# Kernel tuning notes

Measured on AMD Instinct MI355X. Metric: run time of the kernel, lower is better.

Reference implementation:

```python
import jax, jax.numpy as jnp
import numpy as np

B, N, FD, FH, FW = 2, 6, 256, 28, 60
DIM, HEADS, DH = 128, 4, 32
BH, BW = 50, 50
IMG_H, IMG_W = 224, 480
SCALE = DH ** -0.5


def _ln(t, g, b):
    m = t.mean(-1, keepdims=True)
    v = jnp.mean((t - m) ** 2, -1, keepdims=True)
    return (t - m) / jnp.sqrt(v + 1e-5) * g + b


def _bn_relu(t, g, b, m, v):
    # eval-mode BatchNorm2d over channel axis 2 of (b,n,C,h,w), then ReLU
    sh = (1, 1, -1, 1, 1)
    y = (t - m.reshape(sh)) / jnp.sqrt(v.reshape(sh) + 1e-5) * g.reshape(sh) + b.reshape(sh)
    return jax.nn.relu(y)


def setup_inputs():
    key = jax.random.key(0)
    it = iter(jax.random.split(key, 48))
    def rn(shape, s=1.0):
        return s * jax.random.normal(next(it), shape, dtype=jnp.float32)
    # BEVEmbedding.grid buffer: V_inv @ scaled unit grid (first 2 rows used)
    gx, gy = np.meshgrid(np.linspace(0, 1, BW), np.linspace(0, 1, BH))
    grid = np.stack([gx * 200.0, gy * 200.0, np.ones_like(gx)], 0)
    V = np.array([[0.0, -2.0, 100.0], [-2.0, 0.0, 100.0], [0.0, 0.0, 1.0]])
    g = np.linalg.inv(V) @ grid.reshape(3, -1)
    bev_grid = jnp.asarray(g[:2].reshape(2, BH, BW), jnp.float32)
    # image_plane buffer, flattened to (3, fh*fw)
    px, py = np.meshgrid(np.linspace(0, 1, FW) * IMG_W, np.linspace(0, 1, FH) * IMG_H)
    image_plane = jnp.asarray(np.stack([px, py, np.ones_like(px)], 0).reshape(3, -1), jnp.float32)
    ones = jnp.ones(DIM, jnp.float32)
    zeros = jnp.zeros(DIM, jnp.float32)
    return dict(
        x=rn((B, DIM, BH, BW)),
        feature=rn((B, N, FD, FH, FW)),
        I_inv=rn((B, N, 3, 3), 0.01) + jnp.eye(3, dtype=jnp.float32),
        E_inv=rn((B, N, 4, 4), 0.1) + jnp.eye(4, dtype=jnp.float32),
        bev_grid=bev_grid, image_plane=image_plane,
        W_cam=rn((DIM, 4), 0.1), W_img=rn((DIM, 4), 0.1),
        W_bev=rn((DIM, 2), 0.1), b_bev=rn((DIM,), 0.1),
        fp_bn_g=jnp.ones(FD, jnp.float32), fp_bn_b=jnp.zeros(FD, jnp.float32),
        fp_bn_m=rn((FD,), 0.1), fp_bn_v=jax.random.uniform(next(it), (FD,), jnp.float32, 0.5, 1.5),
        fl_bn_g=jnp.ones(FD, jnp.float32), fl_bn_b=jnp.zeros(FD, jnp.float32),
        fl_bn_m=rn((FD,), 0.1), fl_bn_v=jax.random.uniform(next(it), (FD,), jnp.float32, 0.5, 1.5),
        W_fproj=rn((DIM, FD), 0.05), W_flin=rn((DIM, FD), 0.05),
        q_ln_g=ones, q_ln_b=zeros, Wq=rn((HEADS * DH, DIM), 0.05), bq=zeros,
        k_ln_g=ones, k_ln_b=zeros, Wk=rn((HEADS * DH, DIM), 0.05), bk=zeros,
        v_ln_g=ones, v_ln_b=zeros, Wv=rn((HEADS * DH, DIM), 0.05), bv=zeros,
        Wproj=rn((DIM, HEADS * DH), 0.05), bproj=zeros,
        pre_ln_g=ones, pre_ln_b=zeros,
        mlp_W1=rn((2 * DIM, DIM), 0.05), mlp_b1=jnp.zeros(2 * DIM, jnp.float32),
        mlp_W2=rn((DIM, 2 * DIM), 0.05), mlp_b2=zeros,
        post_ln_g=ones, post_ln_b=zeros,
    )


def reference(x, feature, I_inv, E_inv, bev_grid, image_plane, W_cam, W_img, W_bev, b_bev,
              fp_bn_g, fp_bn_b, fp_bn_m, fp_bn_v, fl_bn_g, fl_bn_b, fl_bn_m, fl_bn_v,
              W_fproj, W_flin, q_ln_g, q_ln_b, Wq, bq, k_ln_g, k_ln_b, Wk, bk,
              v_ln_g, v_ln_b, Wv, bv, Wproj, bproj, pre_ln_g, pre_ln_b,
              mlp_W1, mlp_b1, mlp_W2, mlp_b2, post_ln_g, post_ln_b):
    b, n, _, fh, fw = feature.shape
    H, W = x.shape[2], x.shape[3]
    Q, K = H * W, fh * fw
    # camera-center embedding: 1x1 conv on E_inv translation column (b,n,4)
    c_embed = jnp.einsum('dc,bnc->bnd', W_cam, E_inv[..., 3])
    # per-pixel ray directions: E_inv @ pad(I_inv @ pixel, 1)
    cam = jnp.einsum('bnij,jp->bnip', I_inv, image_plane)                 # (b,n,3,K)
    cam = jnp.concatenate([cam, jnp.ones_like(cam[:, :, :1])], axis=2)    # (b,n,4,K)
    d = jnp.einsum('bnij,bnjp->bnip', E_inv, cam)                         # (b,n,4,K)
    img = jnp.einsum('dc,bncp->bndp', W_img, d) - c_embed[..., None]      # (b,n,dim,K)
    img = img / (jnp.linalg.norm(img, axis=2, keepdims=True) + 1e-7)
    # BEV positional embedding (1x1 conv with bias on world grid)
    w_embed = jnp.einsum('dc,chw->dhw', W_bev, bev_grid) + b_bev[:, None, None]
    bev_e = w_embed[None, None] - c_embed[..., None, None]                # (b,n,dim,H,W)
    bev_e = bev_e / (jnp.linalg.norm(bev_e, axis=2, keepdims=True) + 1e-7)
    # key/value features: BN(eval)+ReLU+1x1 conv
    key_feat = jnp.einsum('dc,bnchw->bndhw', W_fproj, _bn_relu(feature, fp_bn_g, fp_bn_b, fp_bn_m, fp_bn_v))
    key = img.reshape(b, n, -1, fh, fw) + key_feat                        # (b,n,dim,fh,fw)
    val = jnp.einsum('dc,bnchw->bndhw', W_flin, _bn_relu(feature, fl_bn_g, fl_bn_b, fl_bn_m, fl_bn_v))
    query = bev_e + x[:, None]                                            # (b,n,dim,H,W)
    # CrossAttention: LN + linear projections
    qx = query.reshape(b, n, -1, Q).transpose(0, 1, 3, 2)                 # (b,n,Q,dim)
    kx = key.reshape(b, n, -1, K).transpose(0, 1, 3, 2)                   # (b,n,K,dim)
    vx = val.reshape(b, n, -1, K).transpose(0, 1, 3, 2).reshape(b, n * K, -1)
    qh = (_ln(qx, q_ln_g, q_ln_b) @ Wq.T + bq).reshape(b, n, Q, HEADS, DH)
    kh = (_ln(kx, k_ln_g, k_ln_b) @ Wk.T + bk).reshape(b, n, K, HEADS, DH)
    vh = (_ln(vx, v_ln_g, v_ln_b) @ Wv.T + bv).reshape(b, n * K, HEADS, DH)
    # scores per view, softmax over flattened (n K) key axis
    dot = SCALE * jnp.einsum('bnqmd,bnkmd->bmqnk', qh, kh)                # (b,m,Q,n,K)
    att = jax.nn.softmax(dot.reshape(b, HEADS, Q, n * K), axis=-1)
    a = jnp.einsum('bmqk,bkmd->bqmd', att, vh).reshape(b, Q, HEADS * DH)
    z = a @ Wproj.T + bproj
    z = z + x.reshape(b, -1, Q).transpose(0, 2, 1)                        # skip connection
    z = _ln(z, pre_ln_g, pre_ln_b)
    z = z + (jax.nn.gelu(z @ mlp_W1.T + mlp_b1, approximate=False) @ mlp_W2.T + mlp_b2)
    z = _ln(z, post_ln_g, post_ln_b)
    return z.transpose(0, 2, 1).reshape(b, -1, H, W)
```

## Files before the change

### kernel.cpp

```cpp
#include <hip/hip_runtime.h>

#define NB    2
#define NCAM  6
#define FD    256
#define KK    1680
#define DIMN  128
#define NHEAD 4
#define DHD   32
#define QQ    2500
#define SCALE 0.17677669529663687f
#define QSCALE ((float)(0.17677669529663687 * 1.4426950408889634))

typedef short bf8 __attribute__((ext_vector_type(8)));
typedef float f4  __attribute__((ext_vector_type(4)));

__device__ __forceinline__ unsigned short f2bf(float f) {
  unsigned int u = __float_as_uint(f);
  unsigned int r = (u + 0x7fffu + ((u >> 16) & 1u)) >> 16;
  return (unsigned short)r;
}

__device__ __forceinline__ float blk_sum128(float v, float* red) {
  #pragma unroll
  for (int o = 32; o > 0; o >>= 1) v += __shfl_down(v, o);
  int t = threadIdx.x;
  if ((t & 63) == 0) red[t >> 6] = v;
  __syncthreads();
  float r = red[0] + red[1];
  __syncthreads();
  return r;
}

__global__ void k_cembed(const float* __restrict__ W_cam, const float* __restrict__ E_inv,
                         float* __restrict__ ce) {
  int bn = blockIdx.x;
  int d  = threadIdx.x;
  const float* e = E_inv + bn * 16;
  float s = 0.f;
  #pragma unroll
  for (int c = 0; c < 4; ++c) s += W_cam[d * 4 + c] * e[c * 4 + 3];
  ce[bn * 128 + d] = s;
}

__global__ void k_img(const float* __restrict__ I_inv, const float* __restrict__ E_inv,
                      const float* __restrict__ plane, const float* __restrict__ W_img,
                      const float* __restrict__ ce, float* __restrict__ key) {
  __shared__ float red[2];
  int p  = blockIdx.x;
  int bn = blockIdx.y;
  int d  = threadIdx.x;
  const float* Ii = I_inv + bn * 9;
  const float* Ei = E_inv + bn * 16;
  float pl0 = plane[p], pl1 = plane[KK + p], pl2 = plane[2 * KK + p];
  float c0 = Ii[0]*pl0 + Ii[1]*pl1 + Ii[2]*pl2;
  float c1 = Ii[3]*pl0 + Ii[4]*pl1 + Ii[5]*pl2;
  float c2 = Ii[6]*pl0 + Ii[7]*pl1 + Ii[8]*pl2;
  float d0 = Ei[0]*c0 + Ei[1]*c1 + Ei[2]*c2  + Ei[3];
  float d1 = Ei[4]*c0 + Ei[5]*c1 + Ei[6]*c2  + Ei[7];
  float d2 = Ei[8]*c0 + Ei[9]*c1 + Ei[10]*c2 + Ei[11];
  float d3 = Ei[12]*c0 + Ei[13]*c1 + Ei[14]*c2 + Ei[15];
  float v = W_img[d*4]*d0 + W_img[d*4+1]*d1 + W_img[d*4+2]*d2 + W_img[d*4+3]*d3
            - ce[bn * 128 + d];
  float ss = blk_sum128(v * v, red);
  float inv = 1.f / (sqrtf(ss) + 1e-7f);
  key[((size_t)bn * KK + p) * DIMN + d] = v * inv;
}

__global__ void k_query(const float* __restrict__ bev_grid, const float* __restrict__ W_bev,
                        const float* __restrict__ b_bev, const float* __restrict__ ce,
                        const float* __restrict__ x, float* __restrict__ query) {
  __shared__ float red[2];
  int q  = blockIdx.x;
  int bn = blockIdx.y;
  int b  = bn / NCAM;
  int d  = threadIdx.x;
  float g0 = bev_grid[q], g1 = bev_grid[QQ + q];
  float v = W_bev[d * 2] * g0 + W_bev[d * 2 + 1] * g1 + b_bev[d] - ce[bn * 128 + d];
  float ss = blk_sum128(v * v, red);
  float inv = 1.f / (sqrtf(ss) + 1e-7f);
  query[((size_t)bn * QQ + q) * DIMN + d] = v * inv + x[(size_t)(b * DIMN + d) * QQ + q];
}

#define TP 16
__global__ void k_featconv(const float* __restrict__ feat,
                           const float* __restrict__ g1c, const float* __restrict__ b1c,
                           const float* __restrict__ m1c, const float* __restrict__ v1c,
                           const float* __restrict__ g2c, const float* __restrict__ b2c,
                           const float* __restrict__ m2c, const float* __restrict__ v2c,
                           const float* __restrict__ Wfp, const float* __restrict__ Wfl,
                           float* __restrict__ key, float* __restrict__ val) {
  __shared__ float sc1[FD], sh1[FD], sc2[FD], sh2[FD];
  __shared__ float t1[FD * (TP + 1)];
  __shared__ float t2[FD * (TP + 1)];
  int tile = blockIdx.x;
  int bn   = blockIdx.y;
  int t    = threadIdx.x;
  int p0   = tile * TP;
  {
    int c = t;
    float s1 = g1c[c] * rsqrtf(v1c[c] + 1e-5f);
    sc1[c] = s1; sh1[c] = b1c[c] - m1c[c] * s1;
    float s2 = g2c[c] * rsqrtf(v2c[c] + 1e-5f);
    sc2[c] = s2; sh2[c] = b2c[c] - m2c[c] * s2;
  }
  __syncthreads();
  const float* fb = feat + (size_t)bn * FD * KK + p0;
  int pp = t & 15, crow = t >> 4;
  #pragma unroll
  for (int i = 0; i < 16; ++i) {
    int c = i * 16 + crow;
    float raw = fb[(size_t)c * KK + pp];
    t1[c * (TP + 1) + pp] = fmaxf(raw * sc1[c] + sh1[c], 0.f);
    t2[c * (TP + 1) + pp] = fmaxf(raw * sc2[c] + sh2[c], 0.f);
  }
  __syncthreads();
  int dd = t & 127;
  const float4* W4 = (const float4*)((t < 128) ? Wfp : Wfl) + dd * 64;
  const float* tl = (t < 128) ? t1 : t2;
  float acc[TP];
  #pragma unroll
  for (int p = 0; p < TP; ++p) acc[p] = 0.f;
  for (int c4 = 0; c4 < 64; ++c4) {
    float4 w = W4[c4];
    const float* r0 = &tl[(c4 * 4 + 0) * (TP + 1)];
    const float* r1 = &tl[(c4 * 4 + 1) * (TP + 1)];
    const float* r2 = &tl[(c4 * 4 + 2) * (TP + 1)];
    const float* r3 = &tl[(c4 * 4 + 3) * (TP + 1)];
    #pragma unroll
    for (int p = 0; p < TP; ++p)
      acc[p] += w.x * r0[p] + w.y * r1[p] + w.z * r2[p] + w.w * r3[p];
  }
  __syncthreads();
  {
    float* dst = (t < 128) ? t1 : t2;
    #pragma unroll
    for (int p = 0; p < TP; ++p) dst[dd * (TP + 1) + p] = acc[p];
  }
  __syncthreads();
  #pragma unroll
  for (int i = 0; i < 16; ++i) {
    int e   = i * 256 + t;
    int ddo = e & 127, po = (e >> 7) & 15, wh = e >> 11;
    size_t addr = ((size_t)bn * KK + p0 + po) * DIMN + ddo;
    float vv = (wh ? t2 : t1)[ddo * (TP + 1) + po];
    if (wh) val[addr] = vv;
    else    key[addr] += vv;
  }
}

#define ROWS 8
template<int MODE>
__global__ void k_lnproj_bf(const float* __restrict__ in, const float* __restrict__ lng,
                            const float* __restrict__ lnb, const float* __restrict__ W,
                            const float* __restrict__ bias, unsigned short* __restrict__ out,
                            float scale) {
  __shared__ float red[2];
  __shared__ float ln[ROWS][DIMN];
  __shared__ float stats[ROWS][2];
  size_t r0 = (size_t)blockIdx.x * ROWS;
  int t = threadIdx.x;
  float g = lng[t], bb = lnb[t];
  float xv[ROWS];
  #pragma unroll
  for (int r = 0; r < ROWS; ++r) xv[r] = in[(r0 + r) * DIMN + t];
  #pragma unroll
  for (int r = 0; r < ROWS; ++r) {
    float s  = blk_sum128(xv[r], red);
    float s2 = blk_sum128(xv[r] * xv[r], red);
    if (t == 0) { stats[r][0] = s * (1.f / 128.f); stats[r][1] = s2 * (1.f / 128.f); }
  }
  __syncthreads();
  #pragma unroll
  for (int r = 0; r < ROWS; ++r) {
    float mu  = stats[r][0];
    float var = fmaxf(stats[r][1] - mu * mu, 0.f);
    float rin = rsqrtf(var + 1e-5f);
    ln[r][t] = (xv[r] - mu) * rin * g + bb;
  }
  __syncthreads();
  float acc[ROWS];
  float bv = bias[t];
  #pragma unroll
  for (int r = 0; r < ROWS; ++r) acc[r] = bv;
  const float4* W4 = (const float4*)W + t * 32;
  for (int j4 = 0; j4 < 32; ++j4) {
    float4 w = W4[j4];
    #pragma unroll
    for (int r = 0; r < ROWS; ++r)
      acc[r] += w.x * ln[r][j4*4] + w.y * ln[r][j4*4+1] + w.z * ln[r][j4*4+2] + w.w * ln[r][j4*4+3];
  }
  if (MODE == 0) {
    #pragma unroll
    for (int r = 0; r < ROWS; ++r) out[(r0 + r) * DIMN + t] = f2bf(acc[r] * scale);
  } else {
    int bn = (int)(r0 / KK), k0 = (int)(r0 % KK);
    int m = t >> 5, d = t & 31;
    unsigned int u0 = (unsigned int)f2bf(acc[0]) | ((unsigned int)f2bf(acc[1]) << 16);
    unsigned int u1 = (unsigned int)f2bf(acc[2]) | ((unsigned int)f2bf(acc[3]) << 16);
    unsigned int u2 = (unsigned int)f2bf(acc[4]) | ((unsigned int)f2bf(acc[5]) << 16);
    unsigned int u3 = (unsigned int)f2bf(acc[6]) | ((unsigned int)f2bf(acc[7]) << 16);
    uint4 pk = make_uint4(u0, u1, u2, u3);
    *(uint4*)&out[((size_t)((bn * 4 + m) * 32 + d)) * KK + k0] = pk;
  }
}

#define AW 8
#define NCHUNK 53
#define THR 8.0f
__global__ __launch_bounds__(512)
void k_attn_mfma(const unsigned short* __restrict__ qhB, const unsigned short* __restrict__ khB,
                 const unsigned short* __restrict__ vhB, float* __restrict__ aout) {
  __shared__ unsigned short pls[AW][16 * 40];
  __shared__ float lds_o[AW][16][32];
  __shared__ float lds_m[AW][16], lds_l[AW][16];
  int qt = blockIdx.x, m = blockIdx.y, b = blockIdx.z;
  int t = threadIdx.x;
  int w = t >> 6, l = t & 63;
  int c = l & 15, g = l >> 4;
  int q0 = qt * 16;

  bf8 qf[NCAM];
  #pragma unroll
  for (int n = 0; n < NCAM; ++n) {
    int q = q0 + c;
    if (q < QQ)
      qf[n] = *(const bf8*)&qhB[((size_t)(b * NCAM + n) * QQ + q) * DIMN + m * DHD + g * 8];
    else
      qf[n] = (bf8)0;
  }
  const f4 z4 = {0.f, 0.f, 0.f, 0.f};
  f4 o0 = z4, o1 = z4;
  float mrun[4], lp[4];
  #pragma unroll
  for (int i = 0; i < 4; ++i) { mrun[i] = -1e30f; lp[i] = 0.f; }

  for (int n = 0; n < NCAM; ++n) {
    const unsigned short* kb = khB + (size_t)(b * NCAM + n) * KK * DIMN + m * DHD;
    const unsigned short* vb = vhB + (size_t)((b * NCAM + n) * NHEAD + m) * DHD * KK;
    bf8 qa = qf[n];
    for (int j = w; j < NCHUNK; j += AW) {
      int k0 = j * 32;
      bool tail = (j == NCHUNK - 1);
      bf8 kf0 = *(const bf8*)&kb[(size_t)(k0 + c) * DIMN + g * 8];
      bf8 vf0 = *(const bf8*)&vb[(size_t)c * KK + k0 + g * 8];
      bf8 vf1 = *(const bf8*)&vb[(size_t)(16 + c) * KK + k0 + g * 8];
      f4 s0 = __builtin_amdgcn_mfma_f32_16x16x32_bf16(qa, kf0, z4, 0, 0, 0);
      f4 s1;
      if (!tail) {
        bf8 kf1 = *(const bf8*)&kb[(size_t)(k0 + 16 + c) * DIMN + g * 8];
        s1 = __builtin_amdgcn_mfma_f32_16x16x32_bf16(qa, kf1, z4, 0, 0, 0);
      } else {
        s1 = (f4){-1e30f, -1e30f, -1e30f, -1e30f};
      }
      float lm[4];
      #pragma unroll
      for (int i = 0; i < 4; ++i) lm[i] = fmaxf(s0[i], s1[i]);
      bool ok = (lm[0] <= mrun[0] + THR) && (lm[1] <= mrun[1] + THR)
             && (lm[2] <= mrun[2] + THR) && (lm[3] <= mrun[3] + THR);
      if (!__all(ok)) {
        #pragma unroll
        for (int i = 0; i < 4; ++i) {
          float tm = lm[i];
          #pragma unroll
          for (int msk = 1; msk < 16; msk <<= 1) tm = fmaxf(tm, __shfl_xor(tm, msk, 16));
          float mn = fmaxf(mrun[i], tm);
          float al = __builtin_amdgcn_exp2f(mrun[i] - mn);
          mrun[i] = mn;
          lp[i] *= al;
          o0[i] *= al; o1[i] *= al;
        }
      }
      #pragma unroll
      for (int i = 0; i < 4; ++i) {
        float p0 = __builtin_amdgcn_exp2f(s0[i] - mrun[i]);
        float p1 = __builtin_amdgcn_exp2f(s1[i] - mrun[i]);
        lp[i] += p0 + p1;
        pls[w][(4 * g + i) * 40 + c]      = f2bf(p0);
        pls[w][(4 * g + i) * 40 + 16 + c] = f2bf(p1);
      }
      bf8 pa = *(const bf8*)&pls[w][c * 40 + g * 8];
      o0 = __builtin_amdgcn_mfma_f32_16x16x32_bf16(pa, vf0, o0, 0, 0, 0);
      o1 = __builtin_amdgcn_mfma_f32_16x16x32_bf16(pa, vf1, o1, 0, 0, 0);
    }
  }
  #pragma unroll
  for (int i = 0; i < 4; ++i) {
    #pragma unroll
    for (int msk = 1; msk < 16; msk <<= 1) lp[i] += __shfl_xor(lp[i], msk, 16);
  }
  #pragma unroll
  for (int i = 0; i < 4; ++i) {
    int qr = 4 * g + i;
    if (c == 0) { lds_m[w][qr] = mrun[i]; lds_l[w][qr] = lp[i]; }
    lds_o[w][qr][c]      = o0[i];
    lds_o[w][qr][16 + c] = o1[i];
  }
  __syncthreads();
  {
    int q = t >> 5, d = t & 31;
    float mg = -1e30f;
    #pragma unroll
    for (int ww = 0; ww < AW; ++ww) mg = fmaxf(mg, lds_m[ww][q]);
    float lg = 0.f, og = 0.f;
    #pragma unroll
    for (int ww = 0; ww < AW; ++ww) {
      float sc = __builtin_amdgcn_exp2f(lds_m[ww][q] - mg);
      lg += lds_l[ww][q] * sc;
      og += lds_o[ww][q][d] * sc;
    }
    int qq = q0 + q;
    if (qq < QQ)
      aout[((size_t)b * QQ + qq) * DIMN + m * DHD + d] = og / lg;
  }
}

#define EQ 16
#define EPAD 4
__global__ __launch_bounds__(256)
void k_epi2(const float* __restrict__ a, const float* __restrict__ x,
            const float* __restrict__ Wproj, const float* __restrict__ bproj,
            const float* __restrict__ preg, const float* __restrict__ preb,
            const float* __restrict__ W1, const float* __restrict__ b1,
            const float* __restrict__ W2, const float* __restrict__ b2,
            const float* __restrict__ postg, const float* __restrict__ postb,
            float* __restrict__ out) {
  __shared__ float sa[EQ][DIMN + EPAD];
  __shared__ float sx[EQ][DIMN + EPAD];
  __shared__ float sln[EQ][DIMN + EPAD];
  __shared__ float sh[EQ][2 * DIMN];
  __shared__ float stats[EQ][2];
  int q0 = blockIdx.x * EQ;
  int b  = blockIdx.y;
  int t  = threadIdx.x;
  int d  = t & 127, rg = t >> 7;

  #pragma unroll
  for (int i = 0; i < 8; ++i) {
    int e = i * 256 + t;
    int q = e >> 7, dd = e & 127;
    int qq = q0 + q;
    sa[q][dd] = (qq < QQ) ? a[((size_t)b * QQ + qq) * DIMN + dd] : 0.f;
  }
  #pragma unroll
  for (int i = 0; i < 8; ++i) {
    int e = i * 256 + t;
    int dd = e >> 4, qi = e & 15;
    int qq = q0 + qi;
    sx[qi][dd] = (qq < QQ) ? x[((size_t)b * DIMN + dd) * QQ + qq] : 0.f;
  }
  __syncthreads();

  float z[8];
  {
    const float4* Wp = (const float4*)Wproj + d * 32;
    float bp = bproj[d];
    #pragma unroll
    for (int r = 0; r < 8; ++r) z[r] = bp + sx[rg * 8 + r][d];
    for (int c4 = 0; c4 < 32; ++c4) {
      float4 w = Wp[c4];
      #pragma unroll
      for (int r = 0; r < 8; ++r) {
        float4 av = *(const float4*)&sa[rg * 8 + r][c4 * 4];
        z[r] += w.x * av.x + w.y * av.y + w.z * av.z + w.w * av.w;
      }
    }
  }
  __syncthreads();
  #pragma unroll
  for (int r = 0; r < 8; ++r) sx[rg * 8 + r][d] = z[r];
  __syncthreads();
  {
    int rt = t >> 4, lane = t & 15;
    float s = 0.f, s2 = 0.f;
    #pragma unroll
    for (int j = 0; j < 8; ++j) { float v = sx[rt][lane + 16 * j]; s += v; s2 += v * v; }
    #pragma unroll
    for (int msk = 1; msk < 16; msk <<= 1) { s += __shfl_xor(s, msk, 16); s2 += __shfl_xor(s2, msk, 16); }
    if (lane == 0) { stats[rt][0] = s * (1.f / 128.f); stats[rt][1] = s2 * (1.f / 128.f); }
  }
  __syncthreads();
  float ln1[8];
  {
    float pg = preg[d], pb = preb[d];
    #pragma unroll
    for (int r = 0; r < 8; ++r) {
      int rr = rg * 8 + r;
      float mu  = stats[rr][0];
      float var = fmaxf(stats[rr][1] - mu * mu, 0.f);
      ln1[r] = (z[r] - mu) * rsqrtf(var + 1e-5f) * pg + pb;
      sln[rr][d] = ln1[r];
    }
  }
  __syncthreads();
  {
    const float4* W1p = (const float4*)W1 + t * 32;
    float hb = b1[t];
    float h[16];
    #pragma unroll
    for (int r = 0; r < 16; ++r) h[r] = hb;
    for (int c4 = 0; c4 < 32; ++c4) {
      float4 w = W1p[c4];
      #pragma unroll
      for (int r = 0; r < 16; ++r) {
        float4 lv = *(const float4*)&sln[r][c4 * 4];
        h[r] += w.x * lv.x + w.y * lv.y + w.z * lv.z + w.w * lv.w;
      }
    }
    #pragma unroll
    for (int r = 0; r < 16; ++r) {
      float hv = h[r];
      sh[r][t] = 0.5f * hv * (1.f + erff(hv * 0.70710678118f));
    }
  }
  __syncthreads();
  float o[8];
  {
    const float4* W2p = (const float4*)W2 + d * 64;
    float b2v = b2[d];
    #pragma unroll
    for (int r = 0; r < 8; ++r) o[r] = ln1[r] + b2v;
    for (int c4 = 0; c4 < 64; ++c4) {
      float4 w = W2p[c4];
      #pragma unroll
      for (int r = 0; r < 8; ++r) {
        float4 hv = *(const float4*)&sh[rg * 8 + r][c4 * 4];
        o[r] += w.x * hv.x + w.y * hv.y + w.z * hv.z + w.w * hv.w;
      }
    }
  }
  __syncthreads();
  #pragma unroll
  for (int r = 0; r < 8; ++r) sx[rg * 8 + r][d] = o[r];
  __syncthreads();
  {
    int rt = t >> 4, lane = t & 15;
    float s = 0.f, s2 = 0.f;
    #pragma unroll
    for (int j = 0; j < 8; ++j) { float v = sx[rt][lane + 16 * j]; s += v; s2 += v * v; }
    #pragma unroll
    for (int msk = 1; msk < 16; msk <<= 1) { s += __shfl_xor(s, msk, 16); s2 += __shfl_xor(s2, msk, 16); }
    if (lane == 0) { stats[rt][0] = s * (1.f / 128.f); stats[rt][1] = s2 * (1.f / 128.f); }
  }
  __syncthreads();
  {
    float pg = postg[d], pb = postb[d];
    #pragma unroll
    for (int r = 0; r < 8; ++r) {
      int rr = rg * 8 + r;
      float mu  = stats[rr][0];
      float var = fmaxf(stats[rr][1] - mu * mu, 0.f);
      sa[rr][d] = (o[r] - mu) * rsqrtf(var + 1e-5f) * pg + pb;
    }
  }
  __syncthreads();
  #pragma unroll
  for (int i = 0; i < 8; ++i) {
    int e = i * 256 + t;
    int dd = e >> 4, qi = e & 15;
    int qq = q0 + qi;
    if (qq < QQ) out[((size_t)b * DIMN + dd) * QQ + qq] = sa[qi][dd];
  }
}

extern "C" void kernel_launch(void* const* d_in, const int* in_sizes, int n_in,
                              void* d_out, int out_size, void* d_ws, size_t ws_size,
                              hipStream_t stream) {
  const float* x        = (const float*)d_in[0];
  const float* feature  = (const float*)d_in[1];
  const float* I_inv    = (const float*)d_in[2];
  const float* E_inv    = (const float*)d_in[3];
  const float* bev_grid = (const float*)d_in[4];
  const float* plane    = (const float*)d_in[5];
  const float* W_cam    = (const float*)d_in[6];
  const float* W_img    = (const float*)d_in[7];
  const float* W_bev    = (const float*)d_in[8];
  const float* b_bev    = (const float*)d_in[9];
  const float* fp_g = (const float*)d_in[10];
  const float* fp_b = (const float*)d_in[11];
  const float* fp_m = (const float*)d_in[12];
  const float* fp_v = (const float*)d_in[13];
  const float* fl_g = (const float*)d_in[14];
  const float* fl_b = (const float*)d_in[15];
  const float* fl_m = (const float*)d_in[16];
  const float* fl_v = (const float*)d_in[17];
  const float* W_fproj = (const float*)d_in[18];
  const float* W_flin  = (const float*)d_in[19];
  const float* q_ln_g = (const float*)d_in[20];
  const float* q_ln_b = (const float*)d_in[21];
  const float* Wq = (const float*)d_in[22];
  const float* bq = (const float*)d_in[23];
  const float* k_ln_g = (const float*)d_in[24];
  const float* k_ln_b = (const float*)d_in[25];
  const float* Wk = (const float*)d_in[26];
  const float* bk = (const float*)d_in[27];
  const float* v_ln_g = (const float*)d_in[28];
  const float* v_ln_b = (const float*)d_in[29];
  const float* Wv = (const float*)d_in[30];
  const float* bv = (const float*)d_in[31];
  const float* Wproj = (const float*)d_in[32];
  const float* bproj = (const float*)d_in[33];
  const float* pre_g = (const float*)d_in[34];
  const float* pre_b = (const float*)d_in[35];
  const float* W1 = (const float*)d_in[36];
  const float* b1 = (const float*)d_in[37];
  const float* W2 = (const float*)d_in[38];
  const float* b2 = (const float*)d_in[39];
  const float* post_g = (const float*)d_in[40];
  const float* post_b = (const float*)d_in[41];

  float* ws    = (float*)d_ws;
  float* ce    = ws;
  float* keyb  = ce + 2048;
  float* valb  = keyb + 2580480;
  float* query = valb + 2580480;
  float* aout  = query + 3840000;
  unsigned short* qhB = (unsigned short*)(aout + 640000);
  unsigned short* vhB = qhB + 3840000;
  unsigned short* khB = vhB + 2580480;

  k_cembed<<<12, 128, 0, stream>>>(W_cam, E_inv, ce);
  k_img<<<dim3(KK, 12), 128, 0, stream>>>(I_inv, E_inv, plane, W_img, ce, keyb);
  k_query<<<dim3(QQ, 12), 128, 0, stream>>>(bev_grid, W_bev, b_bev, ce, x, query);
  k_featconv<<<dim3(KK / TP, 12), 256, 0, stream>>>(feature,
      fp_g, fp_b, fp_m, fp_v, fl_g, fl_b, fl_m, fl_v, W_fproj, W_flin, keyb, valb);
  k_lnproj_bf<0><<<(12 * QQ) / ROWS, 128, 0, stream>>>(query, q_ln_g, q_ln_b, Wq, bq, qhB, QSCALE);
  k_lnproj_bf<0><<<(12 * KK) / ROWS, 128, 0, stream>>>(keyb, k_ln_g, k_ln_b, Wk, bk, khB, 1.0f);
  k_lnproj_bf<1><<<(12 * KK) / ROWS, 128, 0, stream>>>(valb, v_ln_g, v_ln_b, Wv, bv, vhB, 1.0f);
  k_attn_mfma<<<dim3((QQ + 15) / 16, NHEAD, NB), 512, 0, stream>>>(qhB, khB, vhB, aout);
  k_epi2<<<dim3((QQ + EQ - 1) / EQ, NB), 256, 0, stream>>>(aout, x, Wproj, bproj,
      pre_g, pre_b, W1, b1, W2, b2, post_g, post_b, (float*)d_out);
}
```

Measured before the change: 581.2 us.

## Move feature conv and LN projections to bf16 MFMA with pre-converted weights

Replaces the scalar fp32 feature 1x1-conv kernel and the three LayerNorm+linear projection kernels with bf16 MFMA versions that work on 64-row tiles. A new small kernel converts the five weight matrices to bf16 on every call. The LN stats are now computed per row with quad shuffles instead of block reductions, and the V output is transposed through shared memory. This cuts FP32 ALU time in the pre-attention stages, at the cost of bf16 rounding of activations and weights in the conv and an extra launch.

```diff
diff --git a/kernel.cpp b/kernel.cpp
--- a/kernel.cpp
+++ b/kernel.cpp
@@ -29,6 +29,27 @@
   float r = red[0] + red[1];
   __syncthreads();
   return r;
+}
+
+__global__ __launch_bounds__(256)
+void k_cvtw(const float* __restrict__ a0, const float* __restrict__ a1,
+            const float* __restrict__ a2, const float* __restrict__ a3,
+            const float* __restrict__ a4,
+            unsigned short* __restrict__ b0, unsigned short* __restrict__ b1,
+            unsigned short* __restrict__ b2, unsigned short* __restrict__ b3,
+            unsigned short* __restrict__ b4) {
+  int bid = blockIdx.x;
+  const float* s; unsigned short* d; int off;
+  if (bid < 32)      { s = a0; d = b0; off = bid; }
+  else if (bid < 64) { s = a1; d = b1; off = bid - 32; }
+  else if (bid < 80) { s = a2; d = b2; off = bid - 64; }
+  else if (bid < 96) { s = a3; d = b3; off = bid - 80; }
+  else               { s = a4; d = b4; off = bid - 96; }
+  int i = off * 1024 + threadIdx.x * 4;
+  float4 v = *(const float4*)&s[i];
+  uint2 pk = make_uint2((unsigned)f2bf(v.x) | ((unsigned)f2bf(v.y) << 16),
+                        (unsigned)f2bf(v.z) | ((unsigned)f2bf(v.w) << 16));
+  *(uint2*)&d[i] = pk;
 }
 
 __global__ void k_cembed(const float* __restrict__ W_cam, const float* __restrict__ E_inv,
@@ -81,126 +102,167 @@
   query[((size_t)bn * QQ + q) * DIMN + d] = v * inv + x[(size_t)(b * DIMN + d) * QQ + q];
 }
 
-#define TP 16
-__global__ void k_featconv(const float* __restrict__ feat,
-                           const float* __restrict__ g1c, const float* __restrict__ b1c,
-                           const float* __restrict__ m1c, const float* __restrict__ v1c,
-                           const float* __restrict__ g2c, const float* __restrict__ b2c,
-                           const float* __restrict__ m2c, const float* __restrict__ v2c,
-                           const float* __restrict__ Wfp, const float* __restrict__ Wfl,
-                           float* __restrict__ key, float* __restrict__ val) {
-  __shared__ float sc1[FD], sh1[FD], sc2[FD], sh2[FD];
-  __shared__ float t1[FD * (TP + 1)];
-  __shared__ float t2[FD * (TP + 1)];
-  int tile = blockIdx.x;
-  int bn   = blockIdx.y;
-  int t    = threadIdx.x;
-  int p0   = tile * TP;
-  {
-    int c = t;
-    float s1 = g1c[c] * rsqrtf(v1c[c] + 1e-5f);
-    sc1[c] = s1; sh1[c] = b1c[c] - m1c[c] * s1;
-    float s2 = g2c[c] * rsqrtf(v2c[c] + 1e-5f);
-    sc2[c] = s2; sh2[c] = b2c[c] - m2c[c] * s2;
-  }
-  __syncthreads();
-  const float* fb = feat + (size_t)bn * FD * KK + p0;
-  int pp = t & 15, crow = t >> 4;
-  #pragma unroll
-  for (int i = 0; i < 16; ++i) {
-    int c = i * 16 + crow;
-    float raw = fb[(size_t)c * KK + pp];
-    t1[c * (TP + 1) + pp] = fmaxf(raw * sc1[c] + sh1[c], 0.f);
-    t2[c * (TP + 1) + pp] = fmaxf(raw * sc2[c] + sh2[c], 0.f);
-  }
-  __syncthreads();
-  int dd = t & 127;
-  const float4* W4 = (const float4*)((t < 128) ? Wfp : Wfl) + dd * 64;
-  const float* tl = (t < 128) ? t1 : t2;
-  float acc[TP];
-  #pragma unroll
-  for (int p = 0; p < TP; ++p) acc[p] = 0.f;
-  for (int c4 = 0; c4 < 64; ++c4) {
-    float4 w = W4[c4];
-    const float* r0 = &tl[(c4 * 4 + 0) * (TP + 1)];
-    const float* r1 = &tl[(c4 * 4 + 1) * (TP + 1)];
-    const float* r2 = &tl[(c4 * 4 + 2) * (TP + 1)];
-    const float* r3 = &tl[(c4 * 4 + 3) * (TP + 1)];
-    #pragma unroll
-    for (int p = 0; p < TP; ++p)
-      acc[p] += w.x * r0[p] + w.y * r1[p] + w.z * r2[p] + w.w * r3[p];
-  }
-  __syncthreads();
-  {
-    float* dst = (t < 128) ? t1 : t2;
-    #pragma unroll
-    for (int p = 0; p < TP; ++p) dst[dd * (TP + 1) + p] = acc[p];
-  }
-  __syncthreads();
-  #pragma unroll
-  for (int i = 0; i < 16; ++i) {
-    int e   = i * 256 + t;
-    int ddo = e & 127, po = (e >> 7) & 15, wh = e >> 11;
-    size_t addr = ((size_t)bn * KK + p0 + po) * DIMN + ddo;
-    float vv = (wh ? t2 : t1)[ddo * (TP + 1) + po];
-    if (wh) val[addr] = vv;
-    else    key[addr] += vv;
-  }
-}
-
-#define ROWS 8
+#define FTP 64
+#define FSTR 264
+__global__ __launch_bounds__(256)
+void k_featconv_mfma(const float* __restrict__ feat,
+                     const float* __restrict__ g1c, const float* __restrict__ b1c,
+                     const float* __restrict__ m1c, const float* __restrict__ v1c,
+                     const float* __restrict__ g2c, const float* __restrict__ b2c,
+                     const float* __restrict__ m2c, const float* __restrict__ v2c,
+                     const unsigned short* __restrict__ WfpB,
+                     const unsigned short* __restrict__ WflB,
+                     float* __restrict__ key, float* __restrict__ val) {
+  __shared__ unsigned short act[FTP * FSTR];
+  __shared__ float scs[2][FD], shs[2][FD];
+  int tile = blockIdx.x, bn = blockIdx.y;
+  int p0 = tile * FTP;
+  int t = threadIdx.x;
+  {
+    float s1 = g1c[t] * rsqrtf(v1c[t] + 1e-5f);
+    scs[0][t] = s1; shs[0][t] = b1c[t] - m1c[t] * s1;
+    float s2 = g2c[t] * rsqrtf(v2c[t] + 1e-5f);
+    scs[1][t] = s2; shs[1][t] = b2c[t] - m2c[t] * s2;
+  }
+  int w = t >> 6, l = t & 63, c = l & 15, g = l >> 4;
+  const float* fb = feat + (size_t)bn * FD * KK;
+  for (int var = 0; var < 2; ++var) {
+    __syncthreads();
+    #pragma unroll
+    for (int it = 0; it < 16; ++it) {
+      int e   = it * 256 + t;
+      int cin = e >> 4;
+      int pq  = (e & 15) * 4;
+      int pp  = min(p0 + pq, KK - 4);
+      float4 r = *(const float4*)&fb[(size_t)cin * KK + pp];
+      float s = scs[var][cin], h = shs[var][cin];
+      act[(pq + 0) * FSTR + cin] = f2bf(fmaxf(r.x * s + h, 0.f));
+      act[(pq + 1) * FSTR + cin] = f2bf(fmaxf(r.y * s + h, 0.f));
+      act[(pq + 2) * FSTR + cin] = f2bf(fmaxf(r.z * s + h, 0.f));
+      act[(pq + 3) * FSTR + cin] = f2bf(fmaxf(r.w * s + h, 0.f));
+    }
+    __syncthreads();
+    const unsigned short* W = var ? WflB : WfpB;
+    bf8 af[8];
+    #pragma unroll
+    for (int kk = 0; kk < 8; ++kk)
+      af[kk] = *(const bf8*)&act[(w * 16 + c) * FSTR + kk * 32 + g * 8];
+    f4 acc[8];
+    #pragma unroll
+    for (int grp = 0; grp < 8; ++grp) {
+      f4 a = {0.f, 0.f, 0.f, 0.f};
+      #pragma unroll
+      for (int kk = 0; kk < 8; ++kk) {
+        bf8 bfr = *(const bf8*)&W[(grp * 16 + c) * FD + kk * 32 + g * 8];
+        a = __builtin_amdgcn_mfma_f32_16x16x32_bf16(af[kk], bfr, a, 0, 0, 0);
+      }
+      acc[grp] = a;
+    }
+    #pragma unroll
+    for (int i = 0; i < 4; ++i) {
+      int pos = p0 + w * 16 + 4 * g + i;
+      if (pos < KK) {
+        size_t base = ((size_t)bn * KK + pos) * DIMN + c;
+        if (var == 0) {
+          #pragma unroll
+          for (int grp = 0; grp < 8; ++grp) key[base + grp * 16] += acc[grp][i];
+        } else {
+          #pragma unroll
+          for (int grp = 0; grp < 8; ++grp) val[base + grp * 16] = acc[grp][i];
+        }
+      }
+    }
+  }
+}
+
+#define LSTR 136
 template<int MODE>
-__global__ void k_lnproj_bf(const float* __restrict__ in, const float* __restrict__ lng,
-                            const float* __restrict__ lnb, const float* __restrict__ W,
-                            const float* __restrict__ bias, unsigned short* __restrict__ out,
-                            float scale) {
-  __shared__ float red[2];
-  __shared__ float ln[ROWS][DIMN];
-  __shared__ float stats[ROWS][2];
-  size_t r0 = (size_t)blockIdx.x * ROWS;
+__global__ __launch_bounds__(256)
+void k_lnproj_mfma(const float* __restrict__ in, int nrows,
+                   const float* __restrict__ lng, const float* __restrict__ lnbb,
+                   const unsigned short* __restrict__ WB, const float* __restrict__ bias,
+                   float scale, unsigned short* __restrict__ out) {
+  __shared__ unsigned short lnb[64 * LSTR];
+  int tile = blockIdx.x, bn = blockIdx.y;
   int t = threadIdx.x;
-  float g = lng[t], bb = lnb[t];
-  float xv[ROWS];
-  #pragma unroll
-  for (int r = 0; r < ROWS; ++r) xv[r] = in[(r0 + r) * DIMN + t];
-  #pragma unroll
-  for (int r = 0; r < ROWS; ++r) {
-    float s  = blk_sum128(xv[r], red);
-    float s2 = blk_sum128(xv[r] * xv[r], red);
-    if (t == 0) { stats[r][0] = s * (1.f / 128.f); stats[r][1] = s2 * (1.f / 128.f); }
-  }
-  __syncthreads();
-  #pragma unroll
-  for (int r = 0; r < ROWS; ++r) {
-    float mu  = stats[r][0];
-    float var = fmaxf(stats[r][1] - mu * mu, 0.f);
-    float rin = rsqrtf(var + 1e-5f);
-    ln[r][t] = (xv[r] - mu) * rin * g + bb;
-  }
-  __syncthreads();
-  float acc[ROWS];
-  float bv = bias[t];
-  #pragma unroll
-  for (int r = 0; r < ROWS; ++r) acc[r] = bv;
-  const float4* W4 = (const float4*)W + t * 32;
-  for (int j4 = 0; j4 < 32; ++j4) {
-    float4 w = W4[j4];
-    #pragma unroll
-    for (int r = 0; r < ROWS; ++r)
-      acc[r] += w.x * ln[r][j4*4] + w.y * ln[r][j4*4+1] + w.z * ln[r][j4*4+2] + w.w * ln[r][j4*4+3];
+  int r0loc = tile * 64;
+  int valid = nrows - r0loc; if (valid > 64) valid = 64;
+  size_t gr0 = (size_t)bn * nrows + r0loc;
+  int tk = t >> 2, qr = t & 3;
+  int tkc = (tk < valid) ? tk : (valid - 1);
+  const float* ip = &in[(gr0 + tkc) * DIMN + qr * 32];
+  float xv[32];
+  #pragma unroll
+  for (int j = 0; j < 8; ++j) {
+    float4 v = *(const float4*)&ip[j * 4];
+    xv[j*4] = v.x; xv[j*4+1] = v.y; xv[j*4+2] = v.z; xv[j*4+3] = v.w;
+  }
+  float s = 0.f, s2 = 0.f;
+  #pragma unroll
+  for (int j = 0; j < 32; ++j) { s += xv[j]; s2 += xv[j] * xv[j]; }
+  s  += __shfl_xor(s, 1, 4);  s  += __shfl_xor(s, 2, 4);
+  s2 += __shfl_xor(s2, 1, 4); s2 += __shfl_xor(s2, 2, 4);
+  float mu  = s * (1.f / 128.f);
+  float var = fmaxf(s2 * (1.f / 128.f) - mu * mu, 0.f);
+  float rin = rsqrtf(var + 1e-5f);
+  #pragma unroll
+  for (int j4 = 0; j4 < 8; ++j4) {
+    int d = qr * 32 + j4 * 4;
+    float4 gv = *(const float4*)&lng[d];
+    float4 bv = *(const float4*)&lnbb[d];
+    float l0 = (xv[j4*4+0] - mu) * rin * gv.x + bv.x;
+    float l1 = (xv[j4*4+1] - mu) * rin * gv.y + bv.y;
+    float l2 = (xv[j4*4+2] - mu) * rin * gv.z + bv.z;
+    float l3 = (xv[j4*4+3] - mu) * rin * gv.w + bv.w;
+    uint2 pk = make_uint2((unsigned)f2bf(l0) | ((unsigned)f2bf(l1) << 16),
+                          (unsigned)f2bf(l2) | ((unsigned)f2bf(l3) << 16));
+    *(uint2*)&lnb[tk * LSTR + d] = pk;
+  }
+  __syncthreads();
+  int w = t >> 6, l = t & 63, c = l & 15, g = l >> 4;
+  bf8 af[4];
+  #pragma unroll
+  for (int kk = 0; kk < 4; ++kk)
+    af[kk] = *(const bf8*)&lnb[(w * 16 + c) * LSTR + kk * 32 + g * 8];
+  f4 acc[8];
+  #pragma unroll
+  for (int grp = 0; grp < 8; ++grp) {
+    f4 a = {0.f, 0.f, 0.f, 0.f};
+    #pragma unroll
+    for (int kk = 0; kk < 4; ++kk) {
+      bf8 bfr = *(const bf8*)&WB[(grp * 16 + c) * DIMN + kk * 32 + g * 8];
+      a = __builtin_amdgcn_mfma_f32_16x16x32_bf16(af[kk], bfr, a, 0, 0, 0);
+    }
+    acc[grp] = a;
   }
   if (MODE == 0) {
     #pragma unroll
-    for (int r = 0; r < ROWS; ++r) out[(r0 + r) * DIMN + t] = f2bf(acc[r] * scale);
+    for (int grp = 0; grp < 8; ++grp) {
+      float bv = bias[grp * 16 + c];
+      #pragma unroll
+      for (int i = 0; i < 4; ++i) {
+        int rr = w * 16 + 4 * g + i;
+        if (rr < valid)
+          out[(gr0 + rr) * DIMN + grp * 16 + c] = f2bf((acc[grp][i] + bv) * scale);
+      }
+    }
   } else {
-    int bn = (int)(r0 / KK), k0 = (int)(r0 % KK);
-    int m = t >> 5, d = t & 31;
-    unsigned int u0 = (unsigned int)f2bf(acc[0]) | ((unsigned int)f2bf(acc[1]) << 16);
-    unsigned int u1 = (unsigned int)f2bf(acc[2]) | ((unsigned int)f2bf(acc[3]) << 16);
-    unsigned int u2 = (unsigned int)f2bf(acc[4]) | ((unsigned int)f2bf(acc[5]) << 16);
-    unsigned int u3 = (unsigned int)f2bf(acc[6]) | ((unsigned int)f2bf(acc[7]) << 16);
-    uint4 pk = make_uint4(u0, u1, u2, u3);
-    *(uint4*)&out[((size_t)((bn * 4 + m) * 32 + d)) * KK + k0] = pk;
+    #pragma unroll
+    for (int grp = 0; grp < 8; ++grp) {
+      float bv = bias[grp * 16 + c];
+      #pragma unroll
+      for (int i = 0; i < 4; ++i)
+        lnb[(w * 16 + 4 * g + i) * LSTR + grp * 16 + c] = f2bf(acc[grp][i] + bv);
+    }
+    __syncthreads();
+    #pragma unroll
+    for (int it = 0; it < 32; ++it) {
+      int e = it * 256 + t;
+      int dout = e >> 6, tok = e & 63;
+      if (tok < valid)
+        out[((size_t)(bn * 4 + (dout >> 5)) * 32 + (dout & 31)) * KK + r0loc + tok]
+            = lnb[tok * LSTR + dout];
+    }
   }
 }
 
@@ -517,15 +579,25 @@
   unsigned short* qhB = (unsigned short*)(aout + 640000);
   unsigned short* vhB = qhB + 3840000;
   unsigned short* khB = vhB + 2580480;
-
+  unsigned short* WfpB = khB + 2580480;
+  unsigned short* WflB = WfpB + 32768;
+  unsigned short* WqB  = WflB + 32768;
+  unsigned short* WkB  = WqB + 16384;
+  unsigned short* WvB  = WkB + 16384;
+
+  k_cvtw<<<112, 256, 0, stream>>>(W_fproj, W_flin, Wq, Wk, Wv,
+                                  WfpB, WflB, WqB, WkB, WvB);
   k_cembed<<<12, 128, 0, stream>>>(W_cam, E_inv, ce);
   k_img<<<dim3(KK, 12), 128, 0, stream>>>(I_inv, E_inv, plane, W_img, ce, keyb);
   k_query<<<dim3(QQ, 12), 128, 0, stream>>>(bev_grid, W_bev, b_bev, ce, x, query);
-  k_featconv<<<dim3(KK / TP, 12), 256, 0, stream>>>(feature,
-      fp_g, fp_b, fp_m, fp_v, fl_g, fl_b, fl_m, fl_v, W_fproj, W_flin, keyb, valb);
-  k_lnproj_bf<0><<<(12 * QQ) / ROWS, 128, 0, stream>>>(query, q_ln_g, q_ln_b, Wq, bq, qhB, QSCALE);
-  k_lnproj_bf<0><<<(12 * KK) / ROWS, 128, 0, stream>>>(keyb, k_ln_g, k_ln_b, Wk, bk, khB, 1.0f);
-  k_lnproj_bf<1><<<(12 * KK) / ROWS, 128, 0, stream>>>(valb, v_ln_g, v_ln_b, Wv, bv, vhB, 1.0f);
+  k_featconv_mfma<<<dim3((KK + FTP - 1) / FTP, 12), 256, 0, stream>>>(feature,
+      fp_g, fp_b, fp_m, fp_v, fl_g, fl_b, fl_m, fl_v, WfpB, WflB, keyb, valb);
+  k_lnproj_mfma<0><<<dim3((QQ + 63) / 64, 12), 256, 0, stream>>>(query, QQ,
+      q_ln_g, q_ln_b, WqB, bq, QSCALE, qhB);
+  k_lnproj_mfma<0><<<dim3((KK + 63) / 64, 12), 256, 0, stream>>>(keyb, KK,
+      k_ln_g, k_ln_b, WkB, bk, 1.0f, khB);
+  k_lnproj_mfma<1><<<dim3((KK + 63) / 64, 12), 256, 0, stream>>>(valb, KK,
+      v_ln_g, v_ln_b, WvB, bv, 1.0f, vhB);
   k_attn_mfma<<<dim3((QQ + 15) / 16, NHEAD, NB), 512, 0, stream>>>(qhB, khB, vhB, aout);
   k_epi2<<<dim3((QQ + EQ - 1) / EQ, NB), 256, 0, stream>>>(aout, x, Wproj, bproj,
       pre_g, pre_b, W1, b1, W2, b2, post_g, post_b, (float*)d_out);
```

Result: faster. 497.2 us (-14.5%).
